# Optimization experiments

Measured on AMD Instinct MI355X. Metric: run time of the kernel, lower is better.

## Reference

```python
import jax, jax.numpy as jnp
import numpy as np

B, P = 4, 65536
TD, HID, OUT = 32, 128, 4
RES = 256
NFREQ = 6
CD = 3 * 2 * NFREQ  # frequency encoding out dim


def setup_inputs() -> dict:
    key = jax.random.key(0)
    ks = jax.random.split(key, 12)

    def w(k, shape):
        fan_in = shape[-1]
        return jax.random.normal(k, shape, jnp.float32) / np.sqrt(fan_in)

    return {
        "triplane": jax.random.normal(ks[0], (3 * B, TD, RES, RES), jnp.float32),
        "coords": jax.random.uniform(ks[1], (B, P, 3), jnp.float32),  # inside aabb [-1,1]^3
        "w_in": w(ks[2], (HID, TD + CD)),
        "b_in": jnp.zeros((HID,), jnp.float32),
        "w_skip": w(ks[3], (HID, TD + CD)),
        "b_skip": jnp.zeros((HID,), jnp.float32),
        "w_before": w(ks[4], (2, HID, HID)),
        "b_before": jnp.zeros((2, HID), jnp.float32),
        "w_after": w(ks[5], (2, HID, HID)),
        "b_after": jnp.zeros((2, HID), jnp.float32),
        "w_out": w(ks[6], (OUT, HID)),
        "b_out": jnp.zeros((OUT,), jnp.float32),
    }


@jax.custom_vjp
def trunc_exp(x):
    return jnp.exp(x)


def _trunc_exp_fwd(x):
    return jnp.exp(x), x


def _trunc_exp_bwd(x, g):
    return (g * jnp.exp(jnp.clip(x, -15.0, 15.0)),)


trunc_exp.defvjp(_trunc_exp_fwd, _trunc_exp_bwd)


def grid_sample_bilinear(feat, gx, gy):
    # feat: [N, C, H, W]; gx, gy: [N, Q] in [-1, 1]; align_corners=True, zero padding.
    N, C, H, W = feat.shape
    ix = (gx + 1.0) * 0.5 * (W - 1)
    iy = (gy + 1.0) * 0.5 * (H - 1)
    x0 = jnp.floor(ix)
    y0 = jnp.floor(iy)
    wx1 = ix - x0
    wy1 = iy - y0
    feat_flat = feat.reshape(N, C, H * W)

    def gather(xf, yf):
        xi = xf.astype(jnp.int32)
        yi = yf.astype(jnp.int32)
        valid = ((xi >= 0) & (xi < W) & (yi >= 0) & (yi < H)).astype(feat.dtype)
        xi = jnp.clip(xi, 0, W - 1)
        yi = jnp.clip(yi, 0, H - 1)
        idx = yi * W + xi  # [N, Q]
        g = jnp.take_along_axis(feat_flat, idx[:, None, :], axis=2)  # [N, C, Q]
        return g * valid[:, None, :]

    out = (
        gather(x0, y0) * ((1 - wx1) * (1 - wy1))[:, None, :]
        + gather(x0 + 1, y0) * (wx1 * (1 - wy1))[:, None, :]
        + gather(x0, y0 + 1) * ((1 - wx1) * wy1)[:, None, :]
        + gather(x0 + 1, y0 + 1) * (wx1 * wy1)[:, None, :]
    )
    return out  # [N, C, Q]


def freq_encode(x):
    # x: [B, P, 3] in [0, 1]; NeRF-style frequency encoding (tcnn 'Frequency').
    freqs = (2.0 ** jnp.arange(NFREQ, dtype=x.dtype)) * jnp.pi  # [NFREQ]
    ang = x[..., :, None] * freqs  # [B, P, 3, NFREQ]
    enc = jnp.concatenate([jnp.sin(ang), jnp.cos(ang)], axis=-1)  # [B, P, 3, 2*NFREQ]
    return enc.reshape(x.shape[0], x.shape[1], CD)


def reference(triplane, coords, w_in, b_in, w_skip, b_skip, w_before, b_before,
              w_after, b_after, w_out, b_out):
    aabb_min = jnp.full((3,), -1.0, jnp.float32)
    aabb_max = jnp.full((3,), 1.0, jnp.float32)

    scaled = 2.0 * (coords - aabb_min) / (aabb_max - aabb_min) - 1.0  # [-1,1]
    norm = (coords - aabb_min) / (aabb_max - aabb_min)  # [0,1]
    selector = jnp.all((norm > 0.0) & (norm < 1.0), axis=-1)  # [B, P]

    # planes: xy=(x,y), xz=(x,z), zy=(y,z); stacked per batch -> [3B, P, 2]
    coords_xy = scaled[:, :, (0, 1)]
    coords_xz = scaled[:, :, (0, 2)]
    coords_zy = scaled[:, :, (1, 2)]
    grid = jnp.stack([coords_xy, coords_xz, coords_zy], axis=1).reshape(3 * B, P, 2)

    feats = grid_sample_bilinear(triplane, grid[..., 0], grid[..., 1])  # [3B, TD, P]
    feats = feats.transpose(0, 2, 1).reshape(B, 3, P, TD).sum(axis=1)  # [B, P, TD]

    h = jnp.concatenate([freq_encode(norm), feats], axis=-1)  # [B, P, CD+TD]

    lin = lambda x, w, b: jnp.einsum("bpf,hf->bph", x, w) + b
    x = jax.nn.relu(lin(h, w_in, b_in))
    for i in range(w_before.shape[0]):
        x = jax.nn.relu(lin(x, w_before[i], b_before[i]))
    x = x + jax.nn.relu(lin(h, w_skip, b_skip))
    for i in range(w_after.shape[0]):
        x = jax.nn.relu(lin(x, w_after[i], b_after[i]))
    x = lin(x, w_out, b_out)  # [B, P, 4]

    rgb = jax.nn.sigmoid(x[..., :3])
    density = trunc_exp(x[..., 3:4] - 1.0) * selector[..., None].astype(x.dtype)
    return rgb, density
```

## Files before the change

### kernel.cpp

```cpp
#include <hip/hip_runtime.h>
#include <stdint.h>

typedef short short8 __attribute__((ext_vector_type(8)));
typedef float floatx16 __attribute__((ext_vector_type(16)));
typedef unsigned int uint32;

#define NPTS (4 * 65536)
#define RGB_OFF (NPTS * 3)
#define GTOT (2048 * 256)

__device__ __forceinline__ uint16_t bf_rne(float f) {
  uint32 u = __float_as_uint(f);
  u += 0x7FFFu + ((u >> 16) & 1u);
  return (uint16_t)(u >> 16);
}
__device__ __forceinline__ uint32 pack2(float a, float b) {
  return __builtin_amdgcn_perm(__float_as_uint(b) + 0x8000u,
                               __float_as_uint(a) + 0x8000u, 0x07060302u);
}
__device__ __forceinline__ float bf_lo(uint32 u) { return __uint_as_float(u << 16); }
__device__ __forceinline__ float bf_hi(uint32 u) { return __uint_as_float(u & 0xFFFF0000u); }
__device__ __forceinline__ void swap32(uint32& a, uint32& b) {
  asm("v_permlane32_swap_b32 %0, %1" : "+v"(a), "+v"(b));
}
__device__ __forceinline__ void gacc(const uint16_t* p, float w, float* acc) {
  uint4 q = *(const uint4*)p;
  acc[0] += w * bf_lo(q.x);
  acc[1] += w * bf_hi(q.x);
  acc[2] += w * bf_lo(q.y);
  acc[3] += w * bf_hi(q.y);
  acc[4] += w * bf_lo(q.z);
  acc[5] += w * bf_hi(q.z);
  acc[6] += w * bf_lo(q.w);
  acc[7] += w * bf_hi(q.w);
}

__global__ __launch_bounds__(256) void k_prep(
    const float* __restrict__ tri, uint16_t* __restrict__ out, int ntr,
    const float* __restrict__ w_in, const float* __restrict__ w_skip,
    const float* __restrict__ w_before, const float* __restrict__ w_after,
    const float* __restrict__ w_out, const float* __restrict__ b_in,
    const float* __restrict__ b_skip, const float* __restrict__ b_before,
    const float* __restrict__ b_after, const float* __restrict__ b_out,
    uint16_t* __restrict__ wpack, float* __restrict__ bpack) {
  const int bx = blockIdx.x;
  if (bx < ntr) {
    const size_t P = (size_t)bx * 256 + threadIdx.x;
    const int n = (int)(P >> 16);
    const int rem = (int)(P & 65535);
    const float* src = tri + ((size_t)n << 21) + rem;
    uint32 q[16];
#pragma unroll
    for (int c = 0; c < 16; ++c) {
      float a = src[(size_t)(2 * c) << 16];
      float b = src[(size_t)(2 * c + 1) << 16];
      q[c] = pack2(a, b);
    }
    uint4* dst = (uint4*)(out + P * 32);
    dst[0] = make_uint4(q[0], q[1], q[2], q[3]);
    dst[1] = make_uint4(q[4], q[5], q[6], q[7]);
    dst[2] = make_uint4(q[8], q[9], q[10], q[11]);
    dst[3] = make_uint4(q[12], q[13], q[14], q[15]);
    return;
  }
  const int blk = bx - ntr;
  if (blk >= 44) {
    for (int t = threadIdx.x; t < 800; t += 256) {
      int l, idx;
      if (t < 768) { l = t >> 7; idx = t & 127; }
      else { l = 6; idx = t - 768; }
      int mt = idx >> 5, rem = idx & 31;
      int half = rem >> 4, r = rem & 15;
      int f = mt * 32 + (r & 3) + 8 * (r >> 2) + 4 * half;
      float v;
      switch (l) {
        case 0: v = b_in[f]; break;
        case 1: v = b_before[f]; break;
        case 2: v = b_before[128 + f]; break;
        case 3: v = b_skip[f]; break;
        case 4: v = b_after[f]; break;
        case 5: v = b_after[128 + f]; break;
        default: v = (f < 4) ? b_out[f] : 0.0f; break;
      }
      bpack[l * 128 + idx] = v;
    }
    return;
  }
  const int w = blk * 4 + (threadIdx.x >> 6);
  const int L = threadIdx.x & 63;
  int lay, mt, k;
  if (w < 20)      { lay = 0; mt = w / 5;        k = w - mt * 5; }
  else if (w < 52) { int u = w - 20;  lay = 1; mt = u >> 3; k = u & 7; }
  else if (w < 84) { int u = w - 52;  lay = 2; mt = u >> 3; k = u & 7; }
  else if (w < 104){ int u = w - 84;  lay = 3; mt = u / 5;  k = u - mt * 5; }
  else if (w < 136){ int u = w - 104; lay = 4; mt = u >> 3; k = u & 7; }
  else if (w < 168){ int u = w - 136; lay = 5; mt = u >> 3; k = u & 7; }
  else             { lay = 6; mt = 0; k = w - 168; }
  const float* W;
  int insk = 0;
  switch (lay) {
    case 0: W = w_in; insk = 1; break;
    case 1: W = w_before; break;
    case 2: W = w_before + 16384; break;
    case 3: W = w_skip; insk = 1; break;
    case 4: W = w_after; break;
    case 5: W = w_after + 16384; break;
    default: W = w_out; break;
  }
  const int frow = mt * 32 + (L & 31);
  const int kbase = k * 16 + (L >> 5) * 8;
  uint16_t h[8];
#pragma unroll
  for (int j = 0; j < 8; ++j) {
    int kl = kbase + j;
    float v;
    if (insk) {
      int col = (kl < 32) ? (36 + kl) : ((kl < 68) ? (kl - 32) : -1);
      v = (col < 0) ? 0.0f : W[frow * 68 + col];
    } else if (lay == 6) {
      v = (frow < 4) ? W[frow * 128 + kl] : 0.0f;
    } else {
      v = W[frow * 128 + kl];
    }
    h[j] = bf_rne(v);
  }
  uint4 q;
  q.x = (uint32)h[0] | ((uint32)h[1] << 16);
  q.y = (uint32)h[2] | ((uint32)h[3] << 16);
  q.z = (uint32)h[4] | ((uint32)h[5] << 16);
  q.w = (uint32)h[6] | ((uint32)h[7] << 16);
  *(uint4*)(wpack + (size_t)w * 512 + L * 8) = q;
}

__device__ __forceinline__ void gather_encode(const uint16_t* __restrict__ trit,
                                              const float* __restrict__ coords,
                                              int pg, int kh, uint4* hq,
                                              bool* selp) {
  float cx = coords[pg * 3 + 0], cy = coords[pg * 3 + 1], cz = coords[pg * 3 + 2];
  float f1x = cx + 1.0f, f1y = cy + 1.0f, f1z = cz + 1.0f;
  float nx = f1x * 0.5f, ny = f1y * 0.5f, nz = f1z * 0.5f;
  float sx = f1x - 1.0f, sy = f1y - 1.0f, sz = f1z - 1.0f;
  *selp = (nx > 0.f) & (nx < 1.f) & (ny > 0.f) & (ny < 1.f) & (nz > 0.f) & (nz < 1.f);
  const int b = pg >> 16;
  float acc[16];
#pragma unroll
  for (int j = 0; j < 16; ++j) acc[j] = 0.f;
#pragma unroll
  for (int pl = 0; pl < 3; ++pl) {
    float gx = (pl == 2) ? sy : sx;
    float gy = (pl == 0) ? sy : sz;
    float ix = ((gx + 1.0f) * 0.5f) * 255.0f;
    float iy = ((gy + 1.0f) * 0.5f) * 255.0f;
    float x0f = floorf(ix), y0f = floorf(iy);
    float wx = ix - x0f, wy = iy - y0f;
    float vx0 = (x0f >= 0.0f && x0f < 256.0f) ? 1.f : 0.f;
    float vx1 = (x0f >= -1.0f && x0f < 255.0f) ? 1.f : 0.f;
    float vy0 = (y0f >= 0.0f && y0f < 256.0f) ? 1.f : 0.f;
    float vy1 = (y0f >= -1.0f && y0f < 255.0f) ? 1.f : 0.f;
    int x0 = min(max((int)x0f, 0), 255), x1 = min(max((int)x0f + 1, 0), 255);
    int y0 = min(max((int)y0f, 0), 255), y1 = min(max((int)y0f + 1, 0), 255);
    float w00 = (1.f - wx) * (1.f - wy) * vx0 * vy0;
    float w10 = wx * (1.f - wy) * vx1 * vy0;
    float w01 = (1.f - wx) * wy * vx0 * vy1;
    float w11 = wx * wy * vx1 * vy1;
    const int n = 3 * b + pl;
    const uint16_t* cb = trit + ((size_t)n << 21) + kh * 8;
    size_t o00 = (size_t)(y0 * 256 + x0) << 5, o10 = (size_t)(y0 * 256 + x1) << 5;
    size_t o01 = (size_t)(y1 * 256 + x0) << 5, o11 = (size_t)(y1 * 256 + x1) << 5;
    gacc(cb + o00, w00, acc); gacc(cb + 16 + o00, w00, acc + 8);
    gacc(cb + o10, w10, acc); gacc(cb + 16 + o10, w10, acc + 8);
    gacc(cb + o01, w01, acc); gacc(cb + 16 + o01, w01, acc + 8);
    gacc(cb + o11, w11, acc); gacc(cb + 16 + o11, w11, acc + 8);
  }
  hq[0] = make_uint4(pack2(acc[0], acc[1]), pack2(acc[2], acc[3]),
                     pack2(acc[4], acc[5]), pack2(acc[6], acc[7]));
  hq[1] = make_uint4(pack2(acc[8], acc[9]), pack2(acc[10], acc[11]),
                     pack2(acc[12], acc[13]), pack2(acc[14], acc[15]));
  float sv[3][6], cv[3][6];
#pragma unroll
  for (int d = 0; d < 3; ++d) {
    float nd = (d == 0) ? nx : (d == 1) ? ny : nz;
#pragma unroll
    for (int k = 0; k < 6; ++k) {
      float rev = nd * (0.5f * (float)(1 << k));
      float r = rev - rintf(rev);
      sv[d][k] = __builtin_amdgcn_sinf(r);
      cv[d][k] = __builtin_amdgcn_cosf(r);
    }
  }
  if (kh == 0) {
    hq[2] = make_uint4(pack2(sv[0][0], sv[0][1]), pack2(sv[0][2], sv[0][3]),
                       pack2(sv[0][4], sv[0][5]), pack2(cv[0][0], cv[0][1]));
    hq[3] = make_uint4(pack2(sv[1][4], sv[1][5]), pack2(cv[1][0], cv[1][1]),
                       pack2(cv[1][2], cv[1][3]), pack2(cv[1][4], cv[1][5]));
    hq[4] = make_uint4(pack2(cv[2][2], cv[2][3]), pack2(cv[2][4], cv[2][5]), 0u, 0u);
  } else {
    hq[2] = make_uint4(pack2(cv[0][2], cv[0][3]), pack2(cv[0][4], cv[0][5]),
                       pack2(sv[1][0], sv[1][1]), pack2(sv[1][2], sv[1][3]));
    hq[3] = make_uint4(pack2(sv[2][0], sv[2][1]), pack2(sv[2][2], sv[2][3]),
                       pack2(sv[2][4], sv[2][5]), pack2(cv[2][0], cv[2][1]));
    hq[4] = make_uint4(0u, 0u, 0u, 0u);
  }
}

__global__ __launch_bounds__(256) void k_gather(const uint16_t* __restrict__ trit,
                                                const float* __restrict__ coords,
                                                uint4* __restrict__ hfb) {
  const int t = threadIdx.x;
  const int L = t & 63;
  const int kh = L >> 5;
  const int p = (t >> 6) * 32 + (L & 31);
  const int pg = blockIdx.x * 128 + p;
  const int gid = blockIdx.x * 256 + t;
  uint4 hq[5];
  bool sel;
  gather_encode(trit, coords, pg, kh, hq, &sel);
#pragma unroll
  for (int f = 0; f < 5; ++f) hfb[(size_t)f * GTOT + gid] = hq[f];
}

template <int NFRAG>
__device__ __forceinline__ void stage(const uint16_t* __restrict__ wp_base,
                                      uint16_t* __restrict__ wbuf, int t) {
#pragma unroll
  for (int i = 0; i < NFRAG * 64 / 256; ++i) {
    const int g = t + i * 256;
    uint4 v = *(const uint4*)(wp_base + g * 8);
    *(uint4*)(wbuf + g * 8) = v;
  }
}

template <int LAY, int Ks>
__device__ __forceinline__ void mfma_block(floatx16* a, const short8* bin,
                                           const uint16_t* __restrict__ wbuf,
                                           const float* __restrict__ bpack, int L,
                                           int kh) {
#pragma unroll
  for (int mt = 0; mt < 4; ++mt) {
    const float4* bp = (const float4*)(bpack + LAY * 128 + mt * 32 + kh * 16);
#pragma unroll
    for (int g = 0; g < 4; ++g) {
      float4 v = bp[g];
      a[mt][4 * g + 0] = v.x; a[mt][4 * g + 1] = v.y;
      a[mt][4 * g + 2] = v.z; a[mt][4 * g + 3] = v.w;
    }
  }
  const uint16_t* wp = wbuf + L * 8;
#pragma unroll
  for (int k = 0; k < Ks; ++k) {
    short8 w0 = *(const short8*)(wp + (size_t)(0 * Ks + k) * 512);
    short8 w1 = *(const short8*)(wp + (size_t)(1 * Ks + k) * 512);
    short8 w2 = *(const short8*)(wp + (size_t)(2 * Ks + k) * 512);
    short8 w3 = *(const short8*)(wp + (size_t)(3 * Ks + k) * 512);
    a[0] = __builtin_amdgcn_mfma_f32_32x32x16_bf16(w0, bin[k], a[0], 0, 0, 0);
    a[1] = __builtin_amdgcn_mfma_f32_32x32x16_bf16(w1, bin[k], a[1], 0, 0, 0);
    a[2] = __builtin_amdgcn_mfma_f32_32x32x16_bf16(w2, bin[k], a[2], 0, 0, 0);
    a[3] = __builtin_amdgcn_mfma_f32_32x32x16_bf16(w3, bin[k], a[3], 0, 0, 0);
  }
}

template <int LAY, int Ks>
__device__ __forceinline__ void layer_dense(const short8* bin, short8* bout,
                                            const uint16_t* __restrict__ wbuf,
                                            const float* __restrict__ bpack, int L,
                                            int kh) {
  floatx16 a[4];
  mfma_block<LAY, Ks>(a, bin, wbuf, bpack, L, kh);
#pragma unroll
  for (int f = 0; f < 8; ++f) {
    const int mt = f >> 1, s = f & 1;
    uint32 q0a = pack2(fmaxf(a[mt][8 * s + 0], 0.f), fmaxf(a[mt][8 * s + 1], 0.f));
    uint32 q0b = pack2(fmaxf(a[mt][8 * s + 2], 0.f), fmaxf(a[mt][8 * s + 3], 0.f));
    uint32 q1a = pack2(fmaxf(a[mt][8 * s + 4], 0.f), fmaxf(a[mt][8 * s + 5], 0.f));
    uint32 q1b = pack2(fmaxf(a[mt][8 * s + 6], 0.f), fmaxf(a[mt][8 * s + 7], 0.f));
    swap32(q0a, q1a);
    swap32(q0b, q1b);
    bout[f] = __builtin_bit_cast(short8, make_uint4(q0a, q0b, q1a, q1b));
  }
}

template <int LAY, int Ks>
__device__ __forceinline__ void layer_skip(const short8* hin, short8* bio,
                                           const uint16_t* __restrict__ wbuf,
                                           const float* __restrict__ bpack, int L,
                                           int kh) {
  floatx16 a[4];
  mfma_block<LAY, Ks>(a, hin, wbuf, bpack, L, kh);
#pragma unroll
  for (int f = 0; f < 8; ++f) {
    const int mt = f >> 1, s = f & 1;
    uint4 old = __builtin_bit_cast(uint4, bio[f]);
    uint32 uA = old.x, uB = old.y, uC = old.z, uD = old.w;
    swap32(uA, uC);
    swap32(uB, uD);
    float r0 = fmaxf(a[mt][8 * s + 0], 0.f) + bf_lo(uA);
    float r1 = fmaxf(a[mt][8 * s + 1], 0.f) + bf_hi(uA);
    float r2 = fmaxf(a[mt][8 * s + 2], 0.f) + bf_lo(uB);
    float r3 = fmaxf(a[mt][8 * s + 3], 0.f) + bf_hi(uB);
    float r4 = fmaxf(a[mt][8 * s + 4], 0.f) + bf_lo(uC);
    float r5 = fmaxf(a[mt][8 * s + 5], 0.f) + bf_hi(uC);
    float r6 = fmaxf(a[mt][8 * s + 6], 0.f) + bf_lo(uD);
    float r7 = fmaxf(a[mt][8 * s + 7], 0.f) + bf_hi(uD);
    uint32 q0a = pack2(r0, r1), q0b = pack2(r2, r3);
    uint32 q1a = pack2(r4, r5), q1b = pack2(r6, r7);
    swap32(q0a, q1a);
    swap32(q0b, q1b);
    bio[f] = __builtin_bit_cast(short8, make_uint4(q0a, q0b, q1a, q1b));
  }
}

__device__ __forceinline__ void mlp_body(const short8* hf, bool sel,
                                         const uint16_t* __restrict__ wpack,
                                         const float* __restrict__ bpack,
                                         uint16_t* __restrict__ wbuf,
                                         float* __restrict__ dout, int t, int L,
                                         int kh, int pg) {
  short8 bf[8];
  __syncthreads();
  layer_dense<0, 5>(hf, bf, wbuf, bpack, L, kh);
  __syncthreads(); stage<32>(wpack + (size_t)20 * 512, wbuf, t); __syncthreads();
  layer_dense<1, 8>(bf, bf, wbuf, bpack, L, kh);
  __syncthreads(); stage<32>(wpack + (size_t)52 * 512, wbuf, t); __syncthreads();
  layer_dense<2, 8>(bf, bf, wbuf, bpack, L, kh);
  __syncthreads(); stage<20>(wpack + (size_t)84 * 512, wbuf, t); __syncthreads();
  layer_skip<3, 5>(hf, bf, wbuf, bpack, L, kh);
  __syncthreads(); stage<32>(wpack + (size_t)104 * 512, wbuf, t); __syncthreads();
  layer_dense<4, 8>(bf, bf, wbuf, bpack, L, kh);
  __syncthreads(); stage<32>(wpack + (size_t)136 * 512, wbuf, t); __syncthreads();
  layer_dense<5, 8>(bf, bf, wbuf, bpack, L, kh);
  __syncthreads(); stage<8>(wpack + (size_t)168 * 512, wbuf, t); __syncthreads();

  floatx16 a;
  const float4* bp = (const float4*)(bpack + 768 + kh * 16);
#pragma unroll
  for (int g = 0; g < 4; ++g) {
    float4 v = bp[g];
    a[4 * g + 0] = v.x; a[4 * g + 1] = v.y; a[4 * g + 2] = v.z; a[4 * g + 3] = v.w;
  }
  const uint16_t* wp = wbuf + L * 8;
#pragma unroll
  for (int k = 0; k < 8; ++k) {
    short8 af = *(const short8*)(wp + (size_t)k * 512);
    a = __builtin_amdgcn_mfma_f32_32x32x16_bf16(af, bf[k], a, 0, 0, 0);
  }
  if (kh == 0) {
    const float l2e = 1.44269504f;
    float r0 = 1.0f / (1.0f + exp2f(-l2e * a[0]));
    float r1 = 1.0f / (1.0f + exp2f(-l2e * a[1]));
    float r2 = 1.0f / (1.0f + exp2f(-l2e * a[2]));
    float dens = exp2f((a[3] - 1.0f) * l2e) * (sel ? 1.0f : 0.0f);
    dout[pg * 3 + 0] = r0;
    dout[pg * 3 + 1] = r1;
    dout[pg * 3 + 2] = r2;
    dout[RGB_OFF + pg] = dens;
  }
}

__global__ __launch_bounds__(256, 3) void k_mlp(
    const float* __restrict__ coords, const uint16_t* __restrict__ wpack,
    const float* __restrict__ bpack, const uint4* __restrict__ hfb,
    float* __restrict__ dout) {
  __shared__ __align__(16) uint16_t wbuf[16384];
  const int t = threadIdx.x;
  const int L = t & 63;
  const int kh = L >> 5;
  const int p = (t >> 6) * 32 + (L & 31);
  const int pg = blockIdx.x * 128 + p;
  const int gid = blockIdx.x * 256 + t;

  stage<20>(wpack, wbuf, t);

  short8 hf[5];
#pragma unroll
  for (int f = 0; f < 5; ++f)
    hf[f] = __builtin_bit_cast(short8, hfb[(size_t)f * GTOT + gid]);
  float cx = coords[pg * 3 + 0], cy = coords[pg * 3 + 1], cz = coords[pg * 3 + 2];
  float nx = (cx + 1.0f) * 0.5f, ny = (cy + 1.0f) * 0.5f, nz = (cz + 1.0f) * 0.5f;
  bool sel = (nx > 0.f) & (nx < 1.f) & (ny > 0.f) & (ny < 1.f) & (nz > 0.f) & (nz < 1.f);

  mlp_body(hf, sel, wpack, bpack, wbuf, dout, t, L, kh, pg);
}

__global__ __launch_bounds__(256, 3) void k_main(
    const uint16_t* __restrict__ trit, const float* __restrict__ trif,
    const float* __restrict__ coords, const uint16_t* __restrict__ wpack,
    const float* __restrict__ bpack, float* __restrict__ dout, int fast) {
  __shared__ __align__(16) uint16_t wbuf[16384];
  const int t = threadIdx.x;
  const int L = t & 63;
  const int kh = L >> 5;
  const int p = (t >> 6) * 32 + (L & 31);
  const int pg = blockIdx.x * 128 + p;

  stage<20>(wpack, wbuf, t);

  short8 hf[5];
  bool sel;
  if (fast) {
    uint4 hq[5];
    gather_encode(trit, coords, pg, kh, hq, &sel);
#pragma unroll
    for (int f = 0; f < 5; ++f) hf[f] = __builtin_bit_cast(short8, hq[f]);
  } else {
    float cx = coords[pg * 3 + 0], cy = coords[pg * 3 + 1], cz = coords[pg * 3 + 2];
    float f1x = cx + 1.0f, f1y = cy + 1.0f, f1z = cz + 1.0f;
    float nx = f1x * 0.5f, ny = f1y * 0.5f, nz = f1z * 0.5f;
    float sx = f1x - 1.0f, sy = f1y - 1.0f, sz = f1z - 1.0f;
    sel = (nx > 0.f) & (nx < 1.f) & (ny > 0.f) & (ny < 1.f) & (nz > 0.f) & (nz < 1.f);
    const int b = pg >> 16;
    float acc[16];
#pragma unroll
    for (int j = 0; j < 16; ++j) acc[j] = 0.f;
#pragma unroll
    for (int pl = 0; pl < 3; ++pl) {
      float gx = (pl == 2) ? sy : sx;
      float gy = (pl == 0) ? sy : sz;
      float ix = ((gx + 1.0f) * 0.5f) * 255.0f;
      float iy = ((gy + 1.0f) * 0.5f) * 255.0f;
      float x0f = floorf(ix), y0f = floorf(iy);
      float wx = ix - x0f, wy = iy - y0f;
      float vx0 = (x0f >= 0.0f && x0f < 256.0f) ? 1.f : 0.f;
      float vx1 = (x0f >= -1.0f && x0f < 255.0f) ? 1.f : 0.f;
      float vy0 = (y0f >= 0.0f && y0f < 256.0f) ? 1.f : 0.f;
      float vy1 = (y0f >= -1.0f && y0f < 255.0f) ? 1.f : 0.f;
      int x0 = min(max((int)x0f, 0), 255), x1 = min(max((int)x0f + 1, 0), 255);
      int y0 = min(max((int)y0f, 0), 255), y1 = min(max((int)y0f + 1, 0), 255);
      float w00 = (1.f - wx) * (1.f - wy) * vx0 * vy0;
      float w10 = wx * (1.f - wy) * vx1 * vy0;
      float w01 = (1.f - wx) * wy * vx0 * vy1;
      float w11 = wx * wy * vx1 * vy1;
      const int n = 3 * b + pl;
      const float* basef = trif + (((size_t)n * 32) << 16);
#pragma unroll
      for (int j = 0; j < 8; ++j) {
        const float* c0p = basef + (((size_t)(kh * 8 + j)) << 16);
        const float* c1p = basef + (((size_t)(16 + kh * 8 + j)) << 16);
        acc[j] += w00 * c0p[y0 * 256 + x0] + w10 * c0p[y0 * 256 + x1] +
                  w01 * c0p[y1 * 256 + x0] + w11 * c0p[y1 * 256 + x1];
        acc[8 + j] += w00 * c1p[y0 * 256 + x0] + w10 * c1p[y0 * 256 + x1] +
                      w01 * c1p[y1 * 256 + x0] + w11 * c1p[y1 * 256 + x1];
      }
    }
    hf[0] = __builtin_bit_cast(
        short8, make_uint4(pack2(acc[0], acc[1]), pack2(acc[2], acc[3]),
                           pack2(acc[4], acc[5]), pack2(acc[6], acc[7])));
    hf[1] = __builtin_bit_cast(
        short8, make_uint4(pack2(acc[8], acc[9]), pack2(acc[10], acc[11]),
                           pack2(acc[12], acc[13]), pack2(acc[14], acc[15])));
    float sv[3][6], cv[3][6];
#pragma unroll
    for (int d = 0; d < 3; ++d) {
      float nd = (d == 0) ? nx : (d == 1) ? ny : nz;
#pragma unroll
      for (int k = 0; k < 6; ++k) {
        float rev = nd * (0.5f * (float)(1 << k));
        float r = rev - rintf(rev);
        sv[d][k] = __builtin_amdgcn_sinf(r);
        cv[d][k] = __builtin_amdgcn_cosf(r);
      }
    }
    if (kh == 0) {
      hf[2] = __builtin_bit_cast(
          short8, make_uint4(pack2(sv[0][0], sv[0][1]), pack2(sv[0][2], sv[0][3]),
                             pack2(sv[0][4], sv[0][5]), pack2(cv[0][0], cv[0][1])));
      hf[3] = __builtin_bit_cast(
          short8, make_uint4(pack2(sv[1][4], sv[1][5]), pack2(cv[1][0], cv[1][1]),
                             pack2(cv[1][2], cv[1][3]), pack2(cv[1][4], cv[1][5])));
      hf[4] = __builtin_bit_cast(
          short8, make_uint4(pack2(cv[2][2], cv[2][3]), pack2(cv[2][4], cv[2][5]), 0u, 0u));
    } else {
      hf[2] = __builtin_bit_cast(
          short8, make_uint4(pack2(cv[0][2], cv[0][3]), pack2(cv[0][4], cv[0][5]),
                             pack2(sv[1][0], sv[1][1]), pack2(sv[1][2], sv[1][3])));
      hf[3] = __builtin_bit_cast(
          short8, make_uint4(pack2(sv[2][0], sv[2][1]), pack2(sv[2][2], sv[2][3]),
                             pack2(sv[2][4], sv[2][5]), pack2(cv[2][0], cv[2][1])));
      hf[4] = __builtin_bit_cast(short8, make_uint4(0u, 0u, 0u, 0u));
    }
  }
  mlp_body(hf, sel, wpack, bpack, wbuf, dout, t, L, kh, pg);
}

extern "C" void kernel_launch(void* const* d_in, const int* in_sizes, int n_in,
                              void* d_out, int out_size, void* d_ws, size_t ws_size,
                              hipStream_t stream) {
  const float* tri = (const float*)d_in[0];
  const float* coords = (const float*)d_in[1];
  const float* w_in = (const float*)d_in[2];
  const float* b_in = (const float*)d_in[3];
  const float* w_skip = (const float*)d_in[4];
  const float* b_skip = (const float*)d_in[5];
  const float* w_bef = (const float*)d_in[6];
  const float* b_bef = (const float*)d_in[7];
  const float* w_aft = (const float*)d_in[8];
  const float* b_aft = (const float*)d_in[9];
  const float* w_out = (const float*)d_in[10];
  const float* b_out = (const float*)d_in[11];
  const size_t TRI_B = (size_t)12 * 256 * 256 * 32 * 2;
  const size_t WP_B = (size_t)176 * 1024;
  const size_t BP_B = 3200;
  const size_t HF_B = (size_t)5 * GTOT * 16;
  char* ws = (char*)d_ws;
  const int fast = (ws_size >= TRI_B + WP_B + BP_B) ? 1 : 0;
  const int fast2 = (ws_size >= TRI_B + WP_B + BP_B + HF_B) ? 1 : 0;
  uint16_t* trit;
  uint16_t* wpk;
  float* bpk;
  uint4* hfb = nullptr;
  if (fast) {
    trit = (uint16_t*)ws;
    wpk = (uint16_t*)(ws + TRI_B);
    bpk = (float*)(ws + TRI_B + WP_B);
    hfb = (uint4*)(ws + TRI_B + WP_B + BP_B);
  } else {
    trit = (uint16_t*)ws;
    wpk = (uint16_t*)ws;
    bpk = (float*)(ws + WP_B);
  }
  const int ntr = fast ? 3072 : 0;
  k_prep<<<dim3(ntr + 45), dim3(256), 0, stream>>>(
      tri, trit, ntr, w_in, w_skip, w_bef, w_aft, w_out, b_in, b_skip, b_bef,
      b_aft, b_out, wpk, bpk);
  if (fast2) {
    k_gather<<<dim3(2048), dim3(256), 0, stream>>>(trit, coords, hfb);
    k_mlp<<<dim3(2048), dim3(256), 0, stream>>>(coords, wpk, bpk, hfb,
                                                (float*)d_out);
  } else {
    k_main<<<dim3(2048), dim3(256), 0, stream>>>(trit, tri, coords, wpk, bpk,
                                                 (float*)d_out, fast);
  }
}
```

Before: 288.2 us.

## Fuse gather and MLP into one kernel reading weights directly from global memory

Drops the separate gather kernel and the workspace buffer of encoded features, so gather/encode and the MLP run again in a single fused kernel. Weight fragments are now read straight from the packed global buffer (served by the caches) rather than staged into shared memory layer by layer, which removes the per-layer __syncthreads barriers and the LDS footprint. The cost is repeated global/L2 weight loads per wave and the loss of the split kernels' separate occupancy profiles.

Result: faster. 274.4 us (-4.8%).

```diff
diff --git a/kernel.cpp b/kernel.cpp
--- a/kernel.cpp
+++ b/kernel.cpp
@@ -7,7 +7,6 @@
 
 #define NPTS (4 * 65536)
 #define RGB_OFF (NPTS * 3)
-#define GTOT (2048 * 256)
 
 __device__ __forceinline__ uint16_t bf_rne(float f) {
   uint32 u = __float_as_uint(f);
@@ -203,36 +202,9 @@
   }
 }
 
-__global__ __launch_bounds__(256) void k_gather(const uint16_t* __restrict__ trit,
-                                                const float* __restrict__ coords,
-                                                uint4* __restrict__ hfb) {
-  const int t = threadIdx.x;
-  const int L = t & 63;
-  const int kh = L >> 5;
-  const int p = (t >> 6) * 32 + (L & 31);
-  const int pg = blockIdx.x * 128 + p;
-  const int gid = blockIdx.x * 256 + t;
-  uint4 hq[5];
-  bool sel;
-  gather_encode(trit, coords, pg, kh, hq, &sel);
-#pragma unroll
-  for (int f = 0; f < 5; ++f) hfb[(size_t)f * GTOT + gid] = hq[f];
-}
-
-template <int NFRAG>
-__device__ __forceinline__ void stage(const uint16_t* __restrict__ wp_base,
-                                      uint16_t* __restrict__ wbuf, int t) {
-#pragma unroll
-  for (int i = 0; i < NFRAG * 64 / 256; ++i) {
-    const int g = t + i * 256;
-    uint4 v = *(const uint4*)(wp_base + g * 8);
-    *(uint4*)(wbuf + g * 8) = v;
-  }
-}
-
-template <int LAY, int Ks>
+template <int BASE, int LAY, int Ks>
 __device__ __forceinline__ void mfma_block(floatx16* a, const short8* bin,
-                                           const uint16_t* __restrict__ wbuf,
+                                           const uint16_t* __restrict__ wpack,
                                            const float* __restrict__ bpack, int L,
                                            int kh) {
 #pragma unroll
@@ -245,7 +217,7 @@
       a[mt][4 * g + 2] = v.z; a[mt][4 * g + 3] = v.w;
     }
   }
-  const uint16_t* wp = wbuf + L * 8;
+  const uint16_t* wp = wpack + (size_t)BASE * 512 + L * 8;
 #pragma unroll
   for (int k = 0; k < Ks; ++k) {
     short8 w0 = *(const short8*)(wp + (size_t)(0 * Ks + k) * 512);
@@ -259,13 +231,13 @@
   }
 }
 
-template <int LAY, int Ks>
+template <int BASE, int LAY, int Ks>
 __device__ __forceinline__ void layer_dense(const short8* bin, short8* bout,
-                                            const uint16_t* __restrict__ wbuf,
+                                            const uint16_t* __restrict__ wpack,
                                             const float* __restrict__ bpack, int L,
                                             int kh) {
   floatx16 a[4];
-  mfma_block<LAY, Ks>(a, bin, wbuf, bpack, L, kh);
+  mfma_block<BASE, LAY, Ks>(a, bin, wpack, bpack, L, kh);
 #pragma unroll
   for (int f = 0; f < 8; ++f) {
     const int mt = f >> 1, s = f & 1;
@@ -279,13 +251,13 @@
   }
 }
 
-template <int LAY, int Ks>
+template <int BASE, int LAY, int Ks>
 __device__ __forceinline__ void layer_skip(const short8* hin, short8* bio,
-                                           const uint16_t* __restrict__ wbuf,
+                                           const uint16_t* __restrict__ wpack,
                                            const float* __restrict__ bpack, int L,
                                            int kh) {
   floatx16 a[4];
-  mfma_block<LAY, Ks>(a, hin, wbuf, bpack, L, kh);
+  mfma_block<BASE, LAY, Ks>(a, hin, wpack, bpack, L, kh);
 #pragma unroll
   for (int f = 0; f < 8; ++f) {
     const int mt = f >> 1, s = f & 1;
@@ -312,23 +284,15 @@
 __device__ __forceinline__ void mlp_body(const short8* hf, bool sel,
                                          const uint16_t* __restrict__ wpack,
                                          const float* __restrict__ bpack,
-                                         uint16_t* __restrict__ wbuf,
-                                         float* __restrict__ dout, int t, int L,
-                                         int kh, int pg) {
+                                         float* __restrict__ dout, int L, int kh,
+                                         int pg) {
   short8 bf[8];
-  __syncthreads();
-  layer_dense<0, 5>(hf, bf, wbuf, bpack, L, kh);
-  __syncthreads(); stage<32>(wpack + (size_t)20 * 512, wbuf, t); __syncthreads();
-  layer_dense<1, 8>(bf, bf, wbuf, bpack, L, kh);
-  __syncthreads(); stage<32>(wpack + (size_t)52 * 512, wbuf, t); __syncthreads();
-  layer_dense<2, 8>(bf, bf, wbuf, bpack, L, kh);
-  __syncthreads(); stage<20>(wpack + (size_t)84 * 512, wbuf, t); __syncthreads();
-  layer_skip<3, 5>(hf, bf, wbuf, bpack, L, kh);
-  __syncthreads(); stage<32>(wpack + (size_t)104 * 512, wbuf, t); __syncthreads();
-  layer_dense<4, 8>(bf, bf, wbuf, bpack, L, kh);
-  __syncthreads(); stage<32>(wpack + (size_t)136 * 512, wbuf, t); __syncthreads();
-  layer_dense<5, 8>(bf, bf, wbuf, bpack, L, kh);
-  __syncthreads(); stage<8>(wpack + (size_t)168 * 512, wbuf, t); __syncthreads();
+  layer_dense<0, 0, 5>(hf, bf, wpack, bpack, L, kh);
+  layer_dense<20, 1, 8>(bf, bf, wpack, bpack, L, kh);
+  layer_dense<52, 2, 8>(bf, bf, wpack, bpack, L, kh);
+  layer_skip<84, 3, 5>(hf, bf, wpack, bpack, L, kh);
+  layer_dense<104, 4, 8>(bf, bf, wpack, bpack, L, kh);
+  layer_dense<136, 5, 8>(bf, bf, wpack, bpack, L, kh);
 
   floatx16 a;
   const float4* bp = (const float4*)(bpack + 768 + kh * 16);
@@ -337,7 +301,7 @@
     float4 v = bp[g];
     a[4 * g + 0] = v.x; a[4 * g + 1] = v.y; a[4 * g + 2] = v.z; a[4 * g + 3] = v.w;
   }
-  const uint16_t* wp = wbuf + L * 8;
+  const uint16_t* wp = wpack + (size_t)168 * 512 + L * 8;
 #pragma unroll
   for (int k = 0; k < 8; ++k) {
     short8 af = *(const short8*)(wp + (size_t)k * 512);
@@ -356,43 +320,15 @@
   }
 }
 
-__global__ __launch_bounds__(256, 3) void k_mlp(
+__global__ __launch_bounds__(256, 3) void k_main(
+    const uint16_t* __restrict__ trit, const float* __restrict__ trif,
     const float* __restrict__ coords, const uint16_t* __restrict__ wpack,
-    const float* __restrict__ bpack, const uint4* __restrict__ hfb,
-    float* __restrict__ dout) {
-  __shared__ __align__(16) uint16_t wbuf[16384];
+    const float* __restrict__ bpack, float* __restrict__ dout, int fast) {
   const int t = threadIdx.x;
   const int L = t & 63;
   const int kh = L >> 5;
   const int p = (t >> 6) * 32 + (L & 31);
   const int pg = blockIdx.x * 128 + p;
-  const int gid = blockIdx.x * 256 + t;
-
-  stage<20>(wpack, wbuf, t);
-
-  short8 hf[5];
-#pragma unroll
-  for (int f = 0; f < 5; ++f)
-    hf[f] = __builtin_bit_cast(short8, hfb[(size_t)f * GTOT + gid]);
-  float cx = coords[pg * 3 + 0], cy = coords[pg * 3 + 1], cz = coords[pg * 3 + 2];
-  float nx = (cx + 1.0f) * 0.5f, ny = (cy + 1.0f) * 0.5f, nz = (cz + 1.0f) * 0.5f;
-  bool sel = (nx > 0.f) & (nx < 1.f) & (ny > 0.f) & (ny < 1.f) & (nz > 0.f) & (nz < 1.f);
-
-  mlp_body(hf, sel, wpack, bpack, wbuf, dout, t, L, kh, pg);
-}
-
-__global__ __launch_bounds__(256, 3) void k_main(
-    const uint16_t* __restrict__ trit, const float* __restrict__ trif,
-    const float* __restrict__ coords, const uint16_t* __restrict__ wpack,
-    const float* __restrict__ bpack, float* __restrict__ dout, int fast) {
-  __shared__ __align__(16) uint16_t wbuf[16384];
-  const int t = threadIdx.x;
-  const int L = t & 63;
-  const int kh = L >> 5;
-  const int p = (t >> 6) * 32 + (L & 31);
-  const int pg = blockIdx.x * 128 + p;
-
-  stage<20>(wpack, wbuf, t);
 
   short8 hf[5];
   bool sel;
@@ -478,7 +414,7 @@
       hf[4] = __builtin_bit_cast(short8, make_uint4(0u, 0u, 0u, 0u));
     }
   }
-  mlp_body(hf, sel, wpack, bpack, wbuf, dout, t, L, kh, pg);
+  mlp_body(hf, sel, wpack, bpack, dout, L, kh, pg);
 }
 
 extern "C" void kernel_launch(void* const* d_in, const int* in_sizes, int n_in,
@@ -499,19 +435,15 @@
   const size_t TRI_B = (size_t)12 * 256 * 256 * 32 * 2;
   const size_t WP_B = (size_t)176 * 1024;
   const size_t BP_B = 3200;
-  const size_t HF_B = (size_t)5 * GTOT * 16;
   char* ws = (char*)d_ws;
   const int fast = (ws_size >= TRI_B + WP_B + BP_B) ? 1 : 0;
-  const int fast2 = (ws_size >= TRI_B + WP_B + BP_B + HF_B) ? 1 : 0;
   uint16_t* trit;
   uint16_t* wpk;
   float* bpk;
-  uint4* hfb = nullptr;
   if (fast) {
     trit = (uint16_t*)ws;
     wpk = (uint16_t*)(ws + TRI_B);
     bpk = (float*)(ws + TRI_B + WP_B);
-    hfb = (uint4*)(ws + TRI_B + WP_B + BP_B);
   } else {
     trit = (uint16_t*)ws;
     wpk = (uint16_t*)ws;
@@ -521,12 +453,6 @@
   k_prep<<<dim3(ntr + 45), dim3(256), 0, stream>>>(
       tri, trit, ntr, w_in, w_skip, w_bef, w_aft, w_out, b_in, b_skip, b_bef,
       b_aft, b_out, wpk, bpk);
-  if (fast2) {
-    k_gather<<<dim3(2048), dim3(256), 0, stream>>>(trit, coords, hfb);
-    k_mlp<<<dim3(2048), dim3(256), 0, stream>>>(coords, wpk, bpk, hfb,
-                                                (float*)d_out);
-  } else {
-    k_main<<<dim3(2048), dim3(256), 0, stream>>>(trit, tri, coords, wpk, bpk,
-                                                 (float*)d_out, fast);
-  }
-}
+  k_main<<<dim3(2048), dim3(256), 0, stream>>>(trit, tri, coords, wpk, bpk,
+                                               (float*)d_out, fast);
+}
```

## Fuse gather and MLP into one kernel, split layers into half-tiles for occupancy

Applied to the files above, without the earlier changes.

Drops the separate gather kernel and the workspace buffer for encoded features, so every launch runs the fused k_main path that gathers and encodes in registers before the MLP. Each layer now computes two 32-row output tiles at a time instead of four, which halves the live accumulator registers. Launch bounds are raised from 3 to 4 blocks per SM to use the lower register pressure. The risks are spills or lost MFMA overlap from the smaller tiles, and losing the overlap that the two-kernel split gave.

Result: slower. 299.6 us (+3.9%).

```diff
diff --git a/kernel.cpp b/kernel.cpp
--- a/kernel.cpp
+++ b/kernel.cpp
@@ -7,7 +7,6 @@
 
 #define NPTS (4 * 65536)
 #define RGB_OFF (NPTS * 3)
-#define GTOT (2048 * 256)
 
 __device__ __forceinline__ uint16_t bf_rne(float f) {
   uint32 u = __float_as_uint(f);
@@ -130,6 +129,157 @@
   q.z = (uint32)h[4] | ((uint32)h[5] << 16);
   q.w = (uint32)h[6] | ((uint32)h[7] << 16);
   *(uint4*)(wpack + (size_t)w * 512 + L * 8) = q;
+}
+
+template <int NFRAG>
+__device__ __forceinline__ void stage(const uint16_t* __restrict__ wp_base,
+                                      uint16_t* __restrict__ wbuf, int t) {
+#pragma unroll
+  for (int i = 0; i < NFRAG * 64 / 256; ++i) {
+    const int g = t + i * 256;
+    uint4 v = *(const uint4*)(wp_base + g * 8);
+    *(uint4*)(wbuf + g * 8) = v;
+  }
+}
+
+template <int LAY, int Ks, int MT>
+__device__ __forceinline__ void mfma_pair(floatx16* a, const short8* bin,
+                                          const uint16_t* __restrict__ wbuf,
+                                          const float* __restrict__ bpack, int L,
+                                          int kh) {
+#pragma unroll
+  for (int i = 0; i < 2; ++i) {
+    const float4* bp = (const float4*)(bpack + LAY * 128 + (MT + i) * 32 + kh * 16);
+#pragma unroll
+    for (int g = 0; g < 4; ++g) {
+      float4 v = bp[g];
+      a[i][4 * g + 0] = v.x; a[i][4 * g + 1] = v.y;
+      a[i][4 * g + 2] = v.z; a[i][4 * g + 3] = v.w;
+    }
+  }
+  const uint16_t* wp = wbuf + L * 8;
+#pragma unroll
+  for (int k = 0; k < Ks; ++k) {
+    short8 w0 = *(const short8*)(wp + (size_t)((MT + 0) * Ks + k) * 512);
+    short8 w1 = *(const short8*)(wp + (size_t)((MT + 1) * Ks + k) * 512);
+    a[0] = __builtin_amdgcn_mfma_f32_32x32x16_bf16(w0, bin[k], a[0], 0, 0, 0);
+    a[1] = __builtin_amdgcn_mfma_f32_32x32x16_bf16(w1, bin[k], a[1], 0, 0, 0);
+  }
+}
+
+__device__ __forceinline__ void epi_half(const floatx16* a, short8* out4) {
+#pragma unroll
+  for (int f = 0; f < 4; ++f) {
+    const int i = f >> 1, s = f & 1;
+    uint32 q0a = pack2(fmaxf(a[i][8 * s + 0], 0.f), fmaxf(a[i][8 * s + 1], 0.f));
+    uint32 q0b = pack2(fmaxf(a[i][8 * s + 2], 0.f), fmaxf(a[i][8 * s + 3], 0.f));
+    uint32 q1a = pack2(fmaxf(a[i][8 * s + 4], 0.f), fmaxf(a[i][8 * s + 5], 0.f));
+    uint32 q1b = pack2(fmaxf(a[i][8 * s + 6], 0.f), fmaxf(a[i][8 * s + 7], 0.f));
+    swap32(q0a, q1a);
+    swap32(q0b, q1b);
+    out4[f] = __builtin_bit_cast(short8, make_uint4(q0a, q0b, q1a, q1b));
+  }
+}
+
+__device__ __forceinline__ void epi_skip_half(const floatx16* a, short8* bio4) {
+#pragma unroll
+  for (int f = 0; f < 4; ++f) {
+    const int i = f >> 1, s = f & 1;
+    uint4 old = __builtin_bit_cast(uint4, bio4[f]);
+    uint32 uA = old.x, uB = old.y, uC = old.z, uD = old.w;
+    swap32(uA, uC);
+    swap32(uB, uD);
+    float r0 = fmaxf(a[i][8 * s + 0], 0.f) + bf_lo(uA);
+    float r1 = fmaxf(a[i][8 * s + 1], 0.f) + bf_hi(uA);
+    float r2 = fmaxf(a[i][8 * s + 2], 0.f) + bf_lo(uB);
+    float r3 = fmaxf(a[i][8 * s + 3], 0.f) + bf_hi(uB);
+    float r4 = fmaxf(a[i][8 * s + 4], 0.f) + bf_lo(uC);
+    float r5 = fmaxf(a[i][8 * s + 5], 0.f) + bf_hi(uC);
+    float r6 = fmaxf(a[i][8 * s + 6], 0.f) + bf_lo(uD);
+    float r7 = fmaxf(a[i][8 * s + 7], 0.f) + bf_hi(uD);
+    uint32 q0a = pack2(r0, r1), q0b = pack2(r2, r3);
+    uint32 q1a = pack2(r4, r5), q1b = pack2(r6, r7);
+    swap32(q0a, q1a);
+    swap32(q0b, q1b);
+    bio4[f] = __builtin_bit_cast(short8, make_uint4(q0a, q0b, q1a, q1b));
+  }
+}
+
+template <int LAY, int Ks>
+__device__ __forceinline__ void layer_dense(const short8* bin, short8* bout,
+                                            const uint16_t* __restrict__ wbuf,
+                                            const float* __restrict__ bpack, int L,
+                                            int kh) {
+  floatx16 a[2];
+  short8 t0, t1, t2, t3;
+  mfma_pair<LAY, Ks, 0>(a, bin, wbuf, bpack, L, kh);
+  {
+    short8 tt[4];
+    epi_half(a, tt);
+    t0 = tt[0]; t1 = tt[1]; t2 = tt[2]; t3 = tt[3];
+  }
+  mfma_pair<LAY, Ks, 2>(a, bin, wbuf, bpack, L, kh);
+  epi_half(a, bout + 4);
+  bout[0] = t0; bout[1] = t1; bout[2] = t2; bout[3] = t3;
+}
+
+template <int LAY, int Ks>
+__device__ __forceinline__ void layer_skip(const short8* hin, short8* bio,
+                                           const uint16_t* __restrict__ wbuf,
+                                           const float* __restrict__ bpack, int L,
+                                           int kh) {
+  floatx16 a[2];
+  mfma_pair<LAY, Ks, 0>(a, hin, wbuf, bpack, L, kh);
+  epi_skip_half(a, bio);
+  mfma_pair<LAY, Ks, 2>(a, hin, wbuf, bpack, L, kh);
+  epi_skip_half(a, bio + 4);
+}
+
+__device__ __forceinline__ void mlp_body(const short8* hf, bool sel,
+                                         const uint16_t* __restrict__ wpack,
+                                         const float* __restrict__ bpack,
+                                         uint16_t* __restrict__ wbuf,
+                                         float* __restrict__ dout, int t, int L,
+                                         int kh, int pg) {
+  short8 bf[8];
+  __syncthreads();
+  layer_dense<0, 5>(hf, bf, wbuf, bpack, L, kh);
+  __syncthreads(); stage<32>(wpack + (size_t)20 * 512, wbuf, t); __syncthreads();
+  layer_dense<1, 8>(bf, bf, wbuf, bpack, L, kh);
+  __syncthreads(); stage<32>(wpack + (size_t)52 * 512, wbuf, t); __syncthreads();
+  layer_dense<2, 8>(bf, bf, wbuf, bpack, L, kh);
+  __syncthreads(); stage<20>(wpack + (size_t)84 * 512, wbuf, t); __syncthreads();
+  layer_skip<3, 5>(hf, bf, wbuf, bpack, L, kh);
+  __syncthreads(); stage<32>(wpack + (size_t)104 * 512, wbuf, t); __syncthreads();
+  layer_dense<4, 8>(bf, bf, wbuf, bpack, L, kh);
+  __syncthreads(); stage<32>(wpack + (size_t)136 * 512, wbuf, t); __syncthreads();
+  layer_dense<5, 8>(bf, bf, wbuf, bpack, L, kh);
+  __syncthreads(); stage<8>(wpack + (size_t)168 * 512, wbuf, t); __syncthreads();
+
+  floatx16 a;
+  const float4* bp = (const float4*)(bpack + 768 + kh * 16);
+#pragma unroll
+  for (int g = 0; g < 4; ++g) {
+    float4 v = bp[g];
+    a[4 * g + 0] = v.x; a[4 * g + 1] = v.y; a[4 * g + 2] = v.z; a[4 * g + 3] = v.w;
+  }
+  const uint16_t* wp = wbuf + L * 8;
+#pragma unroll
+  for (int k = 0; k < 8; ++k) {
+    short8 af = *(const short8*)(wp + (size_t)k * 512);
+    a = __builtin_amdgcn_mfma_f32_32x32x16_bf16(af, bf[k], a, 0, 0, 0);
+  }
+  if (kh == 0) {
+    const float l2e = 1.44269504f;
+    float r0 = 1.0f / (1.0f + exp2f(-l2e * a[0]));
+    float r1 = 1.0f / (1.0f + exp2f(-l2e * a[1]));
+    float r2 = 1.0f / (1.0f + exp2f(-l2e * a[2]));
+    float dens = exp2f((a[3] - 1.0f) * l2e) * (sel ? 1.0f : 0.0f);
+    dout[pg * 3 + 0] = r0;
+    dout[pg * 3 + 1] = r1;
+    dout[pg * 3 + 2] = r2;
+    dout[RGB_OFF + pg] = dens;
+  }
 }
 
 __device__ __forceinline__ void gather_encode(const uint16_t* __restrict__ trit,
@@ -203,185 +353,7 @@
   }
 }
 
-__global__ __launch_bounds__(256) void k_gather(const uint16_t* __restrict__ trit,
-                                                const float* __restrict__ coords,
-                                                uint4* __restrict__ hfb) {
-  const int t = threadIdx.x;
-  const int L = t & 63;
-  const int kh = L >> 5;
-  const int p = (t >> 6) * 32 + (L & 31);
-  const int pg = blockIdx.x * 128 + p;
-  const int gid = blockIdx.x * 256 + t;
-  uint4 hq[5];
-  bool sel;
-  gather_encode(trit, coords, pg, kh, hq, &sel);
-#pragma unroll
-  for (int f = 0; f < 5; ++f) hfb[(size_t)f * GTOT + gid] = hq[f];
-}
-
-template <int NFRAG>
-__device__ __forceinline__ void stage(const uint16_t* __restrict__ wp_base,
-                                      uint16_t* __restrict__ wbuf, int t) {
-#pragma unroll
-  for (int i = 0; i < NFRAG * 64 / 256; ++i) {
-    const int g = t + i * 256;
-    uint4 v = *(const uint4*)(wp_base + g * 8);
-    *(uint4*)(wbuf + g * 8) = v;
-  }
-}
-
-template <int LAY, int Ks>
-__device__ __forceinline__ void mfma_block(floatx16* a, const short8* bin,
-                                           const uint16_t* __restrict__ wbuf,
-                                           const float* __restrict__ bpack, int L,
-                                           int kh) {
-#pragma unroll
-  for (int mt = 0; mt < 4; ++mt) {
-    const float4* bp = (const float4*)(bpack + LAY * 128 + mt * 32 + kh * 16);
-#pragma unroll
-    for (int g = 0; g < 4; ++g) {
-      float4 v = bp[g];
-      a[mt][4 * g + 0] = v.x; a[mt][4 * g + 1] = v.y;
-      a[mt][4 * g + 2] = v.z; a[mt][4 * g + 3] = v.w;
-    }
-  }
-  const uint16_t* wp = wbuf + L * 8;
-#pragma unroll
-  for (int k = 0; k < Ks; ++k) {
-    short8 w0 = *(const short8*)(wp + (size_t)(0 * Ks + k) * 512);
-    short8 w1 = *(const short8*)(wp + (size_t)(1 * Ks + k) * 512);
-    short8 w2 = *(const short8*)(wp + (size_t)(2 * Ks + k) * 512);
-    short8 w3 = *(const short8*)(wp + (size_t)(3 * Ks + k) * 512);
-    a[0] = __builtin_amdgcn_mfma_f32_32x32x16_bf16(w0, bin[k], a[0], 0, 0, 0);
-    a[1] = __builtin_amdgcn_mfma_f32_32x32x16_bf16(w1, bin[k], a[1], 0, 0, 0);
-    a[2] = __builtin_amdgcn_mfma_f32_32x32x16_bf16(w2, bin[k], a[2], 0, 0, 0);
-    a[3] = __builtin_amdgcn_mfma_f32_32x32x16_bf16(w3, bin[k], a[3], 0, 0, 0);
-  }
-}
-
-template <int LAY, int Ks>
-__device__ __forceinline__ void layer_dense(const short8* bin, short8* bout,
-                                            const uint16_t* __restrict__ wbuf,
-                                            const float* __restrict__ bpack, int L,
-                                            int kh) {
-  floatx16 a[4];
-  mfma_block<LAY, Ks>(a, bin, wbuf, bpack, L, kh);
-#pragma unroll
-  for (int f = 0; f < 8; ++f) {
-    const int mt = f >> 1, s = f & 1;
-    uint32 q0a = pack2(fmaxf(a[mt][8 * s + 0], 0.f), fmaxf(a[mt][8 * s + 1], 0.f));
-    uint32 q0b = pack2(fmaxf(a[mt][8 * s + 2], 0.f), fmaxf(a[mt][8 * s + 3], 0.f));
-    uint32 q1a = pack2(fmaxf(a[mt][8 * s + 4], 0.f), fmaxf(a[mt][8 * s + 5], 0.f));
-    uint32 q1b = pack2(fmaxf(a[mt][8 * s + 6], 0.f), fmaxf(a[mt][8 * s + 7], 0.f));
-    swap32(q0a, q1a);
-    swap32(q0b, q1b);
-    bout[f] = __builtin_bit_cast(short8, make_uint4(q0a, q0b, q1a, q1b));
-  }
-}
-
-template <int LAY, int Ks>
-__device__ __forceinline__ void layer_skip(const short8* hin, short8* bio,
-                                           const uint16_t* __restrict__ wbuf,
-                                           const float* __restrict__ bpack, int L,
-                                           int kh) {
-  floatx16 a[4];
-  mfma_block<LAY, Ks>(a, hin, wbuf, bpack, L, kh);
-#pragma unroll
-  for (int f = 0; f < 8; ++f) {
-    const int mt = f >> 1, s = f & 1;
-    uint4 old = __builtin_bit_cast(uint4, bio[f]);
-    uint32 uA = old.x, uB = old.y, uC = old.z, uD = old.w;
-    swap32(uA, uC);
-    swap32(uB, uD);
-    float r0 = fmaxf(a[mt][8 * s + 0], 0.f) + bf_lo(uA);
-    float r1 = fmaxf(a[mt][8 * s + 1], 0.f) + bf_hi(uA);
-    float r2 = fmaxf(a[mt][8 * s + 2], 0.f) + bf_lo(uB);
-    float r3 = fmaxf(a[mt][8 * s + 3], 0.f) + bf_hi(uB);
-    float r4 = fmaxf(a[mt][8 * s + 4], 0.f) + bf_lo(uC);
-    float r5 = fmaxf(a[mt][8 * s + 5], 0.f) + bf_hi(uC);
-    float r6 = fmaxf(a[mt][8 * s + 6], 0.f) + bf_lo(uD);
-    float r7 = fmaxf(a[mt][8 * s + 7], 0.f) + bf_hi(uD);
-    uint32 q0a = pack2(r0, r1), q0b = pack2(r2, r3);
-    uint32 q1a = pack2(r4, r5), q1b = pack2(r6, r7);
-    swap32(q0a, q1a);
-    swap32(q0b, q1b);
-    bio[f] = __builtin_bit_cast(short8, make_uint4(q0a, q0b, q1a, q1b));
-  }
-}
-
-__device__ __forceinline__ void mlp_body(const short8* hf, bool sel,
-                                         const uint16_t* __restrict__ wpack,
-                                         const float* __restrict__ bpack,
-                                         uint16_t* __restrict__ wbuf,
-                                         float* __restrict__ dout, int t, int L,
-                                         int kh, int pg) {
-  short8 bf[8];
-  __syncthreads();
-  layer_dense<0, 5>(hf, bf, wbuf, bpack, L, kh);
-  __syncthreads(); stage<32>(wpack + (size_t)20 * 512, wbuf, t); __syncthreads();
-  layer_dense<1, 8>(bf, bf, wbuf, bpack, L, kh);
-  __syncthreads(); stage<32>(wpack + (size_t)52 * 512, wbuf, t); __syncthreads();
-  layer_dense<2, 8>(bf, bf, wbuf, bpack, L, kh);
-  __syncthreads(); stage<20>(wpack + (size_t)84 * 512, wbuf, t); __syncthreads();
-  layer_skip<3, 5>(hf, bf, wbuf, bpack, L, kh);
-  __syncthreads(); stage<32>(wpack + (size_t)104 * 512, wbuf, t); __syncthreads();
-  layer_dense<4, 8>(bf, bf, wbuf, bpack, L, kh);
-  __syncthreads(); stage<32>(wpack + (size_t)136 * 512, wbuf, t); __syncthreads();
-  layer_dense<5, 8>(bf, bf, wbuf, bpack, L, kh);
-  __syncthreads(); stage<8>(wpack + (size_t)168 * 512, wbuf, t); __syncthreads();
-
-  floatx16 a;
-  const float4* bp = (const float4*)(bpack + 768 + kh * 16);
-#pragma unroll
-  for (int g = 0; g < 4; ++g) {
-    float4 v = bp[g];
-    a[4 * g + 0] = v.x; a[4 * g + 1] = v.y; a[4 * g + 2] = v.z; a[4 * g + 3] = v.w;
-  }
-  const uint16_t* wp = wbuf + L * 8;
-#pragma unroll
-  for (int k = 0; k < 8; ++k) {
-    short8 af = *(const short8*)(wp + (size_t)k * 512);
-    a = __builtin_amdgcn_mfma_f32_32x32x16_bf16(af, bf[k], a, 0, 0, 0);
-  }
-  if (kh == 0) {
-    const float l2e = 1.44269504f;
-    float r0 = 1.0f / (1.0f + exp2f(-l2e * a[0]));
-    float r1 = 1.0f / (1.0f + exp2f(-l2e * a[1]));
-    float r2 = 1.0f / (1.0f + exp2f(-l2e * a[2]));
-    float dens = exp2f((a[3] - 1.0f) * l2e) * (sel ? 1.0f : 0.0f);
-    dout[pg * 3 + 0] = r0;
-    dout[pg * 3 + 1] = r1;
-    dout[pg * 3 + 2] = r2;
-    dout[RGB_OFF + pg] = dens;
-  }
-}
-
-__global__ __launch_bounds__(256, 3) void k_mlp(
-    const float* __restrict__ coords, const uint16_t* __restrict__ wpack,
-    const float* __restrict__ bpack, const uint4* __restrict__ hfb,
-    float* __restrict__ dout) {
-  __shared__ __align__(16) uint16_t wbuf[16384];
-  const int t = threadIdx.x;
-  const int L = t & 63;
-  const int kh = L >> 5;
-  const int p = (t >> 6) * 32 + (L & 31);
-  const int pg = blockIdx.x * 128 + p;
-  const int gid = blockIdx.x * 256 + t;
-
-  stage<20>(wpack, wbuf, t);
-
-  short8 hf[5];
-#pragma unroll
-  for (int f = 0; f < 5; ++f)
-    hf[f] = __builtin_bit_cast(short8, hfb[(size_t)f * GTOT + gid]);
-  float cx = coords[pg * 3 + 0], cy = coords[pg * 3 + 1], cz = coords[pg * 3 + 2];
-  float nx = (cx + 1.0f) * 0.5f, ny = (cy + 1.0f) * 0.5f, nz = (cz + 1.0f) * 0.5f;
-  bool sel = (nx > 0.f) & (nx < 1.f) & (ny > 0.f) & (ny < 1.f) & (nz > 0.f) & (nz < 1.f);
-
-  mlp_body(hf, sel, wpack, bpack, wbuf, dout, t, L, kh, pg);
-}
-
-__global__ __launch_bounds__(256, 3) void k_main(
+__global__ __launch_bounds__(256, 4) void k_main(
     const uint16_t* __restrict__ trit, const float* __restrict__ trif,
     const float* __restrict__ coords, const uint16_t* __restrict__ wpack,
     const float* __restrict__ bpack, float* __restrict__ dout, int fast) {
@@ -499,19 +471,15 @@
   const size_t TRI_B = (size_t)12 * 256 * 256 * 32 * 2;
   const size_t WP_B = (size_t)176 * 1024;
   const size_t BP_B = 3200;
-  const size_t HF_B = (size_t)5 * GTOT * 16;
   char* ws = (char*)d_ws;
   const int fast = (ws_size >= TRI_B + WP_B + BP_B) ? 1 : 0;
-  const int fast2 = (ws_size >= TRI_B + WP_B + BP_B + HF_B) ? 1 : 0;
   uint16_t* trit;
   uint16_t* wpk;
   float* bpk;
-  uint4* hfb = nullptr;
   if (fast) {
     trit = (uint16_t*)ws;
     wpk = (uint16_t*)(ws + TRI_B);
     bpk = (float*)(ws + TRI_B + WP_B);
-    hfb = (uint4*)(ws + TRI_B + WP_B + BP_B);
   } else {
     trit = (uint16_t*)ws;
     wpk = (uint16_t*)ws;
@@ -521,12 +489,6 @@
   k_prep<<<dim3(ntr + 45), dim3(256), 0, stream>>>(
       tri, trit, ntr, w_in, w_skip, w_bef, w_aft, w_out, b_in, b_skip, b_bef,
       b_aft, b_out, wpk, bpk);
-  if (fast2) {
-    k_gather<<<dim3(2048), dim3(256), 0, stream>>>(trit, coords, hfb);
-    k_mlp<<<dim3(2048), dim3(256), 0, stream>>>(coords, wpk, bpk, hfb,
-                                                (float*)d_out);
-  } else {
-    k_main<<<dim3(2048), dim3(256), 0, stream>>>(trit, tri, coords, wpk, bpk,
-                                                 (float*)d_out, fast);
-  }
-}
+  k_main<<<dim3(2048), dim3(256), 0, stream>>>(trit, tri, coords, wpk, bpk,
+                                               (float*)d_out, fast);
+}
```
